# Performance work log

Measured on AMD Instinct MI355X. Metric: run time of the kernel, lower is better.

Reference implementation:

```python
import jax, jax.numpy as jnp
import numpy as np

B, T, D, H, J = 64, 128, 768, 256, 128  # batch, tokens, input_dim, span_hidden_dim, top_injection_dim
PRUNING_RATIO = 2.0


def setup_inputs() -> dict:
    key = jax.random.key(0)
    ks = jax.random.split(key, 12)
    def w(k, shape, fan_in):
        return jax.random.normal(k, shape, jnp.float32) / np.sqrt(fan_in)
    return {
        "inputs": jax.random.normal(ks[0], (B, T, D), jnp.float32),
        "input_mask": jnp.ones((B, T), jnp.int32),
        "top_injection_embedding": jax.random.normal(ks[1], (B, J), jnp.float32),
        # SpanRepAssembly: start / end projections
        "W_start": w(ks[2], (D, H), D), "b_start": jnp.zeros((H,), jnp.float32),
        "W_end": w(ks[3], (D, H), D), "b_end": jnp.zeros((H,), jnp.float32),
        # span_scorer: ReLU -> Linear(H,H) -> ReLU -> Linear(H,1)
        "W_s1": w(ks[4], (H, H), H), "b_s1": jnp.zeros((H,), jnp.float32),
        "W_s2": w(ks[5], (H, 1), H), "b_s2": jnp.zeros((1,), jnp.float32),
        # top injection path
        "W_inj": w(ks[6], (J, H), J), "b_inj": jnp.zeros((H,), jnp.float32),
        "W_sec": w(ks[7], (H, H), H), "b_sec": jnp.zeros((H,), jnp.float32),
        "W_pred": w(ks[8], (H, 1), H), "b_pred": jnp.zeros((1,), jnp.float32),
    }


def reference(inputs, input_mask, top_injection_embedding,
              W_start, b_start, W_end, b_end,
              W_s1, b_s1, W_s2, b_s2,
              W_inj, b_inj, W_sec, b_sec, W_pred, b_pred):
    b, t, _ = inputs.shape
    k_spans = int(PRUNING_RATIO * t)
    # SpanRepAssembly: span_hidden[b, (s,e)] = startProj(x_s) + endProj(x_e), s <= e,
    # flattened start-major (matches start_end_range ordering).
    A = inputs @ W_start + b_start                      # [B,T,H]
    E = inputs @ W_end + b_end                          # [B,T,H]
    s_idx, e_idx = jnp.triu_indices(t)                  # N = T(T+1)/2 spans, row-major
    span_hidden = A[:, s_idx] + E[:, e_idx]             # [B,N,H]
    m = input_mask.astype(jnp.float32)
    span_mask = m[:, s_idx] * m[:, e_idx]               # [B,N]
    # span_scorer MLP over all spans
    h = jax.nn.relu(span_hidden) @ W_s1 + b_s1
    scores = (jax.nn.relu(h) @ W_s2 + b_s2)[..., 0]     # [B,N]
    # SpanPruner: mask invalid spans to -inf, top-k, sort indices, gather
    masked_scores = jnp.where(span_mask > 0, scores, -jnp.inf)
    _, top_idx = jax.lax.top_k(masked_scores, k_spans)  # [B,K]
    top_idx = jnp.sort(top_idx, axis=1)
    top_span_hidden = jnp.take_along_axis(span_hidden, top_idx[:, :, None], axis=1)  # [B,K,H]
    top_span_mask = jnp.take_along_axis(span_mask, top_idx, axis=1)[..., None]       # [B,K,1]
    top_span_scores = jnp.take_along_axis(masked_scores, top_idx, axis=1)[..., None] # [B,K,1]
    top_span_scores = jnp.where(jnp.isinf(top_span_scores), -1.0, top_span_scores)
    # top-injection scoring head
    inj = (top_injection_embedding @ W_inj + b_inj)[:, None, :]      # [B,1,H]
    sec = top_span_hidden @ W_sec + b_sec                            # [B,K,H]
    top_span_logits = jax.nn.relu(inj + sec) @ W_pred + b_pred + top_span_scores  # [B,K,1]
    top_span_probs = jax.nn.sigmoid(top_span_logits) * top_span_mask
    return top_span_probs
```

## Files before the change

### kernel.cpp

```cpp
#include <hip/hip_runtime.h>
#include <hip/hip_bf16.h>
#include <math.h>

#define BB 64
#define T 128
#define DD 768
#define H 256
#define JJ 128
#define NSPAN 8256
#define KTOP 256
#define SCAP 1024
#define MARGIN 0.03f

typedef __attribute__((ext_vector_type(8))) short bf16x8;
typedef __attribute__((ext_vector_type(4))) float f32x4;

__device__ inline unsigned short bfrne(float x) {
    unsigned u = __float_as_uint(x);
    return (unsigned short)((u + 0x7FFFu + ((u >> 16) & 1u)) >> 16);
}

__device__ inline unsigned pk2(float x, float y) {
    float2 f; f.x = x; f.y = y;
    __hip_bfloat162 h = __float22bfloat162_rn(f);
    return *reinterpret_cast<unsigned*>(&h);
}

template<int CTRL>
__device__ __forceinline__ float dpp_add16(float v) {
    return v + __int_as_float(__builtin_amdgcn_update_dpp(
        0, __float_as_int(v), CTRL, 0xF, 0xF, true));
}

__global__ __launch_bounds__(256) void prep_proj_kernel(
    const float* __restrict__ X,
    const float* __restrict__ Wa, const float* __restrict__ ba,
    const float* __restrict__ Wb, const float* __restrict__ bb,
    float* __restrict__ AE,
    int* __restrict__ s_idx, int* __restrict__ e_idx,
    const float* __restrict__ W1, unsigned short* __restrict__ Wpk,
    const float* __restrict__ tie, const float* __restrict__ Winj,
    const float* __restrict__ binj, float* __restrict__ injv)
{
    const int blk = blockIdx.x;
    const int t = threadIdx.x;

    if (blk >= 256) {
        const int pblk = blk - 256;
        if (pblk == 0) {
            if (t < T) {
                int s = t;
                int start = s * T - (s * (s - 1)) / 2;
                int len = T - s;
                for (int i = 0; i < len; ++i) {
                    s_idx[start + i] = s;
                    e_idx[start + i] = s + i;
                }
            }
        } else if (pblk <= 256) {
            int idx = (pblk - 1) * 256 + t;
            int j  = idx & 7;
            int l  = (idx >> 3) & 63;
            int kc = (idx >> 9) & 7;
            int ct = idx >> 12;
            int k = kc * 32 + (l >> 4) * 8 + j;
            int n = ct * 16 + (l & 15);
            Wpk[idx] = bfrne(W1[k * 256 + n]);
        } else {
            int b = pblk - 257;
            __shared__ float tb[JJ];
            if (t < JJ) tb[t] = tie[b * JJ + t];
            __syncthreads();
            float a = binj[t];
            for (int j = 0; j < JJ; ++j)
                a = fmaf(tb[j], Winj[j * H + t], a);
            injv[b * H + t] = a;
        }
        return;
    }

    const int px = blk & 63;
    const int cb = blk >> 6;
    const int m0 = px * 128;
    const float* W    = (cb < 2) ? Wa : Wb;
    const float* bias = (cb < 2) ? ba : bb;
    const int wc0 = (cb & 1) * 128;
    const int oc0 = (cb < 2) ? wc0 : (256 + wc0);

    __shared__ __align__(16) float Xs[128 * 36];
    __shared__ __align__(16) float Wl[32 * 140];

    const int tx = t & 15;
    const int ty = t >> 4;
    const int ty7 = ty & 7;
    const int wro = tx * 8 + ((tx >> 2) << 2);

    const int xrow = t >> 1;
    const int xh   = t & 1;
    const int xsw  = (xrow >> 3) & 7;
    const int wrow = t >> 4;
    const int wi   = t & 15;

    float4 xg[4], w0r[2], w1r[2];
    {
        const float* xp = &X[(size_t)(m0 + xrow) * DD];
#pragma unroll
        for (int q = 0; q < 4; ++q)
            xg[q] = *(const float4*)&xp[(2 * q + xh) * 4];
        const float* wp0 = &W[(size_t)wrow * 256 + wc0 + wi * 8];
        w0r[0] = *(const float4*)&wp0[0]; w0r[1] = *(const float4*)&wp0[4];
        const float* wp1 = &W[(size_t)(wrow + 16) * 256 + wc0 + wi * 8];
        w1r[0] = *(const float4*)&wp1[0]; w1r[1] = *(const float4*)&wp1[4];
    }

    float acc[8][8];
#pragma unroll
    for (int i = 0; i < 8; ++i)
#pragma unroll
        for (int j = 0; j < 8; ++j) acc[i][j] = 0.f;

    for (int it = 0; it < 24; ++it) {
        __syncthreads();
#pragma unroll
        for (int q = 0; q < 4; ++q) {
            const int kb = 2 * q + xh;
            *(float4*)&Xs[xrow * 36 + ((kb ^ xsw) << 2)] = xg[q];
        }
        *(float4*)&Wl[wrow * 140 + wro]            = w0r[0];
        *(float4*)&Wl[wrow * 140 + wro + 4]        = w0r[1];
        *(float4*)&Wl[(wrow + 16) * 140 + wro]     = w1r[0];
        *(float4*)&Wl[(wrow + 16) * 140 + wro + 4] = w1r[1];
        __syncthreads();
        if (it + 1 < 24) {
            const int kk = (it + 1) * 32;
            const float* xp = &X[(size_t)(m0 + xrow) * DD + kk];
#pragma unroll
            for (int q = 0; q < 4; ++q)
                xg[q] = *(const float4*)&xp[(2 * q + xh) * 4];
            const float* wp0 = &W[(size_t)(kk + wrow) * 256 + wc0 + wi * 8];
            w0r[0] = *(const float4*)&wp0[0]; w0r[1] = *(const float4*)&wp0[4];
            const float* wp1 = &W[(size_t)(kk + wrow + 16) * 256 + wc0 + wi * 8];
            w1r[0] = *(const float4*)&wp1[0]; w1r[1] = *(const float4*)&wp1[4];
        }
#pragma unroll
        for (int kb = 0; kb < 8; ++kb) {
            float4 xv[8];
#pragma unroll
            for (int r8 = 0; r8 < 8; ++r8)
                xv[r8] = *(const float4*)&Xs[(ty * 8 + r8) * 36 + ((kb ^ ty7) << 2)];
#pragma unroll
            for (int j = 0; j < 4; ++j) {
                const int k = kb * 4 + j;
                float4 wv0 = *(const float4*)&Wl[k * 140 + wro];
                float4 wv1 = *(const float4*)&Wl[k * 140 + wro + 4];
                float wq[8] = {wv0.x, wv0.y, wv0.z, wv0.w, wv1.x, wv1.y, wv1.z, wv1.w};
#pragma unroll
                for (int r8 = 0; r8 < 8; ++r8) {
                    const float xv1 = j == 0 ? xv[r8].x : j == 1 ? xv[r8].y
                                    : j == 2 ? xv[r8].z : xv[r8].w;
#pragma unroll
                    for (int c = 0; c < 8; ++c)
                        acc[r8][c] = fmaf(xv1, wq[c], acc[r8][c]);
                }
            }
        }
    }

    float bq[8];
#pragma unroll
    for (int j = 0; j < 8; ++j) bq[j] = bias[wc0 + tx * 8 + j];
#pragma unroll
    for (int r8 = 0; r8 < 8; ++r8) {
        const size_t row = m0 + ty * 8 + r8;
        float4 o0, o1;
        o0.x = acc[r8][0] + bq[0]; o0.y = acc[r8][1] + bq[1];
        o0.z = acc[r8][2] + bq[2]; o0.w = acc[r8][3] + bq[3];
        o1.x = acc[r8][4] + bq[4]; o1.y = acc[r8][5] + bq[5];
        o1.z = acc[r8][6] + bq[6]; o1.w = acc[r8][7] + bq[7];
        *(float4*)&AE[row * 512 + oc0 + tx * 8]     = o0;
        *(float4*)&AE[row * 512 + oc0 + tx * 8 + 4] = o1;
    }
}

__global__ __launch_bounds__(512, 4) void approx_kernel(
    const float* __restrict__ AE,
    const unsigned short* __restrict__ Wpk,
    const float* __restrict__ bs1, const float* __restrict__ Ws2,
    const float* __restrict__ bs2g,
    const int* __restrict__ s_idx, const int* __restrict__ e_idx,
    const int* __restrict__ maskp,
    float* __restrict__ scores)
{
    const int bid   = blockIdx.x;
    const int r     = bid & 7;
    const int q     = bid >> 3;
    const int g     = q >> 3;
    const int chunk = q & 7;
    const int b     = g * 8 + r;
    const int tile0 = chunk * 65;
    const int tcnt  = (516 - tile0 < 65) ? (516 - tile0) : 65;

    __shared__ __align__(16) unsigned short rshf[2][8][64][8];
    __shared__ float pslice[2][8][16];

    const int t      = threadIdx.x;
    const int w      = t >> 6;
    const int lane   = t & 63;
    const int lrow16 = lane & 15;
    const int quad   = lane >> 4;

    bf16x8 bfr[2][8];
    float b1c[2], w2c[2];
#pragma unroll
    for (int c = 0; c < 2; ++c) {
#pragma unroll
        for (int kc = 0; kc < 8; ++kc)
            bfr[c][kc] = *(const bf16x8*)&Wpk[((((2 * w + c) * 8 + kc) * 64) + lane) * 8];
        int col = (2 * w + c) * 16 + lrow16;
        b1c[c] = bs1[col];
        w2c[c] = Ws2[col];
    }
    const float bs2v = bs2g[0];

    const float* Abase = AE + (size_t)b * T * 512;
    const int sp   = t >> 5;
    const int km   = t & 31;
    const int kc_s = km >> 2;
    const int q_s  = km & 3;
    const int slot = (q_s * 16 + sp + kc_s) & 63;

    {
        int n = tile0 * 16 + sp;
        int s = s_idx[n], e = e_idx[n];
        const float* Ar = Abase + (size_t)s * 512 + km * 8;
        const float* Er = Abase + (size_t)e * 512 + 256 + km * 8;
        float4 a0 = *(const float4*)&Ar[0];
        float4 a1 = *(const float4*)&Ar[4];
        float4 e0 = *(const float4*)&Er[0];
        float4 e1 = *(const float4*)&Er[4];
        uint4 v;
        v.x = pk2(fmaxf(a0.x + e0.x, 0.f), fmaxf(a0.y + e0.y, 0.f));
        v.y = pk2(fmaxf(a0.z + e0.z, 0.f), fmaxf(a0.w + e0.w, 0.f));
        v.z = pk2(fmaxf(a1.x + e1.x, 0.f), fmaxf(a1.y + e1.y, 0.f));
        v.w = pk2(fmaxf(a1.z + e1.z, 0.f), fmaxf(a1.w + e1.w, 0.f));
        *(uint4*)&rshf[0][kc_s][slot][0] = v;
    }
    int s_nx = 0, e_nx = 0;
    if (tcnt > 1) {
        int n = (tile0 + 1) * 16 + sp;
        s_nx = s_idx[n]; e_nx = e_idx[n];
    }
    __syncthreads();

    for (int tt = 0; tt < tcnt; ++tt) {
        const int cur = tt & 1;
        float4 a0, a1, e0, e1;
        const bool pf = (tt + 1 < tcnt);
        if (pf) {
            const float* Ar = Abase + (size_t)s_nx * 512 + km * 8;
            const float* Er = Abase + (size_t)e_nx * 512 + 256 + km * 8;
            a0 = *(const float4*)&Ar[0];
            a1 = *(const float4*)&Ar[4];
            e0 = *(const float4*)&Er[0];
            e1 = *(const float4*)&Er[4];
        }
        if (tt + 2 < tcnt) {
            int n = (tile0 + tt + 2) * 16 + sp;
            s_nx = s_idx[n]; e_nx = e_idx[n];
        }
        f32x4 acc0 = {0.f, 0.f, 0.f, 0.f};
        f32x4 acc1 = {0.f, 0.f, 0.f, 0.f};
#pragma unroll
        for (int kc = 0; kc < 8; ++kc) {
            bf16x8 a = *(const bf16x8*)&rshf[cur][kc][(lane + kc) & 63][0];
            acc0 = __builtin_amdgcn_mfma_f32_16x16x32_bf16(a, bfr[0][kc], acc0, 0, 0, 0);
            acc1 = __builtin_amdgcn_mfma_f32_16x16x32_bf16(a, bfr[1][kc], acc1, 0, 0, 0);
        }
        float ps[4];
#pragma unroll
        for (int rr = 0; rr < 4; ++rr)
            ps[rr] = fmaxf(acc0[rr] + b1c[0], 0.f) * w2c[0]
                   + fmaxf(acc1[rr] + b1c[1], 0.f) * w2c[1];
#pragma unroll
        for (int rr = 0; rr < 4; ++rr) {
            float v = ps[rr];
            v = dpp_add16<0xB1>(v);
            v = dpp_add16<0x4E>(v);
            v = dpp_add16<0x141>(v);
            v = dpp_add16<0x140>(v);
            ps[rr] = v;
        }
        if (lrow16 == 0) {
            float4 v; v.x = ps[0]; v.y = ps[1]; v.z = ps[2]; v.w = ps[3];
            *(float4*)&pslice[cur][w][quad * 4] = v;
        }
        if (pf) {
            uint4 v;
            v.x = pk2(fmaxf(a0.x + e0.x, 0.f), fmaxf(a0.y + e0.y, 0.f));
            v.y = pk2(fmaxf(a0.z + e0.z, 0.f), fmaxf(a0.w + e0.w, 0.f));
            v.z = pk2(fmaxf(a1.x + e1.x, 0.f), fmaxf(a1.y + e1.y, 0.f));
            v.w = pk2(fmaxf(a1.z + e1.z, 0.f), fmaxf(a1.w + e1.w, 0.f));
            *(uint4*)&rshf[cur ^ 1][kc_s][slot][0] = v;
        }
        __syncthreads();
        if (t < 16) {
            int n = (tile0 + tt) * 16 + t;
            float sc = bs2v;
#pragma unroll
            for (int ww = 0; ww < 8; ++ww) sc += pslice[cur][ww][t];
            int s = s_idx[n], e = e_idx[n];
            bool m = (maskp[b * T + s] != 0) && (maskp[b * T + e] != 0);
            scores[(size_t)b * NSPAN + n] = m ? sc : -INFINITY;
        }
    }
}

__global__ __launch_bounds__(1024) void select_kernel(
    const float* __restrict__ scores,
    int* __restrict__ shortlist, int* __restrict__ slcnt)
{
    const int b = blockIdx.x;
    const int t = threadIdx.x;
    __shared__ unsigned su[NSPAN];
    __shared__ int hist[256];
    __shared__ unsigned s_prefix;
    __shared__ int s_remaining;
    __shared__ int wave_keep[16];

    const float* sc = scores + (size_t)b * NSPAN;
    for (int i = t; i < NSPAN; i += 1024) {
        unsigned ub = __float_as_uint(sc[i]);
        su[i] = (ub & 0x80000000u) ? ~ub : (ub | 0x80000000u);
    }
    __syncthreads();

    unsigned prefix = 0;
    int remaining = KTOP;
    for (int d = 3; d >= 0; --d) {
        if (t < 256) hist[t] = 0;
        __syncthreads();
        const int sh = d * 8;
        for (int i = t; i < NSPAN; i += 1024) {
            unsigned u = su[i];
            bool match = (d == 3) || ((u >> (sh + 8)) == (prefix >> (sh + 8)));
            if (match) atomicAdd(&hist[(u >> sh) & 255], 1);
        }
        __syncthreads();
        if (t == 0) {
            int acc = 0, v = 255;
            for (; v > 0; --v) {
                int h = hist[v];
                if (acc + h >= remaining) break;
                acc += h;
            }
            s_prefix = prefix | ((unsigned)v << sh);
            s_remaining = remaining - acc;
        }
        __syncthreads();
        prefix = s_prefix;
        remaining = s_remaining;
        __syncthreads();
    }

    unsigned ub = (prefix & 0x80000000u) ? (prefix & 0x7FFFFFFFu) : ~prefix;
    float kthf = __uint_as_float(ub);
    float tau = kthf - MARGIN;
    unsigned tb = __float_as_uint(tau);
    unsigned ktau = (tb & 0x80000000u) ? ~tb : (tb | 0x80000000u);

    const int wid = t >> 6, lane = t & 63;
    int base = 0;
    const unsigned long long ltmask = (1ull << lane) - 1ull;
    for (int c0 = 0; c0 < NSPAN; c0 += 1024) {
        int n = c0 + t;
        bool keep = (n < NSPAN) && (su[n] >= ktau);
        unsigned long long bk = __ballot(keep);
        int before = __popcll(bk & ltmask);
        if (lane == 0) wave_keep[wid] = __popcll(bk);
        __syncthreads();
        int kb = base;
        for (int wv = 0; wv < wid; ++wv) kb += wave_keep[wv];
        if (keep) {
            int pos = kb + before;
            if (pos < SCAP) shortlist[b * SCAP + pos] = n;
        }
        for (int wv = 0; wv < 16; ++wv) base += wave_keep[wv];
        __syncthreads();
    }
    if (t == 0) slcnt[b] = base < SCAP ? base : SCAP;
}

__global__ __launch_bounds__(512) void exact_kernel(
    const float* __restrict__ AE,
    const float* __restrict__ Ws1, const float* __restrict__ bs1,
    const float* __restrict__ Ws2, const float* __restrict__ bs2g,
    const int* __restrict__ s_idx, const int* __restrict__ e_idx,
    const int* __restrict__ shortlist, const int* __restrict__ slcnt,
    float* __restrict__ scores)
{
    const int b  = blockIdx.y;
    const int n0 = blockIdx.x * 64;
    const int cntb = slcnt[b];
    if (n0 >= cntb) return;

    __shared__ float rsh[64][36];
    __shared__ float Ws[32][260];
    __shared__ int   ss[64], se[64], nn[64];

    const int t = threadIdx.x;
    if (t < 64) {
        int row = n0 + t;
        int n = 0;
        if (row < cntb) n = shortlist[b * SCAP + row];
        nn[t] = (row < cntb) ? n : -1;
        ss[t] = s_idx[n]; se[t] = e_idx[n];
    }
    __syncthreads();

    const int tx = t & 31;
    const int ty = t >> 5;
    float acc[4][8];
#pragma unroll
    for (int i = 0; i < 4; ++i)
#pragma unroll
        for (int j = 0; j < 8; ++j) acc[i][j] = 0.f;

    const float* Abase = AE + (size_t)b * T * 512;

    for (int kk = 0; kk < 256; kk += 32) {
        __syncthreads();
        {
            int row = t >> 4, q4 = (t & 15) * 4;
#pragma unroll
            for (int q = 0; q < 4; ++q)
                *(float4*)&Ws[row][q4 + q * 64] =
                    *(const float4*)&Ws1[(size_t)(kk + row) * 256 + q4 + q * 64];
        }
        {
            int sp = t >> 3, k4 = (t & 7) * 4;
            const float* Ar = Abase + (size_t)ss[sp] * 512 + kk + k4;
            const float* Er = Abase + (size_t)se[sp] * 512 + 256 + kk + k4;
            float4 a = *(const float4*)Ar;
            float4 e = *(const float4*)Er;
            float4 v;
            v.x = fmaxf(a.x + e.x, 0.f); v.y = fmaxf(a.y + e.y, 0.f);
            v.z = fmaxf(a.z + e.z, 0.f); v.w = fmaxf(a.w + e.w, 0.f);
            *(float4*)&rsh[sp][k4] = v;
        }
        __syncthreads();
#pragma unroll
        for (int k4 = 0; k4 < 32; k4 += 4) {
            float w[4][8];
#pragma unroll
            for (int kq = 0; kq < 4; ++kq) {
                float4 w0 = *(const float4*)&Ws[k4 + kq][tx * 4];
                float4 w1 = *(const float4*)&Ws[k4 + kq][128 + tx * 4];
                w[kq][0] = w0.x; w[kq][1] = w0.y; w[kq][2] = w0.z; w[kq][3] = w0.w;
                w[kq][4] = w1.x; w[kq][5] = w1.y; w[kq][6] = w1.z; w[kq][7] = w1.w;
            }
#pragma unroll
            for (int i = 0; i < 4; ++i) {
                float4 rv = *(const float4*)&rsh[ty * 4 + i][k4];
                float rq[4] = {rv.x, rv.y, rv.z, rv.w};
#pragma unroll
                for (int kq = 0; kq < 4; ++kq)
#pragma unroll
                    for (int j = 0; j < 8; ++j)
                        acc[i][j] = fmaf(rq[kq], w[kq][j], acc[i][j]);
            }
        }
    }

    float b1[8], w2[8];
#pragma unroll
    for (int j = 0; j < 8; ++j) {
        int c = (j < 4) ? (tx * 4 + j) : (128 + tx * 4 + j - 4);
        b1[j] = bs1[c];
        w2[j] = Ws2[c];
    }
    const float bs2v = bs2g[0];
#pragma unroll
    for (int i = 0; i < 4; ++i) {
        int r = ty * 4 + i;
        float p = 0.f;
#pragma unroll
        for (int j = 0; j < 8; ++j)
            p += fmaxf(acc[i][j] + b1[j], 0.f) * w2[j];
#pragma unroll
        for (int off = 16; off > 0; off >>= 1)
            p += __shfl_down(p, off, 32);
        if (tx == 0) {
            int n = nn[r];
            if (n >= 0)
                scores[(size_t)b * NSPAN + n] = p + bs2v;
        }
    }
}

__global__ __launch_bounds__(1024) void topk_kernel(
    const float* __restrict__ scores,
    const int* __restrict__ shortlist, const int* __restrict__ slcnt,
    int* __restrict__ top_idx, float* __restrict__ top_scores)
{
    const int b = blockIdx.x;
    const int t = threadIdx.x;
    const int cnt = slcnt[b];

    __shared__ unsigned su[SCAP];
    __shared__ int sn[SCAP];
    __shared__ int hist[256];
    __shared__ unsigned s_prefix;
    __shared__ int s_remaining;
    __shared__ int wave_eq[16], wave_keep[16];

    for (int i = t; i < cnt; i += 1024) {
        int n = shortlist[b * SCAP + i];
        unsigned ub = __float_as_uint(scores[(size_t)b * NSPAN + n]);
        su[i] = (ub & 0x80000000u) ? ~ub : (ub | 0x80000000u);
        sn[i] = n;
    }
    __syncthreads();

    unsigned prefix = 0;
    int remaining = KTOP;
    for (int d = 3; d >= 0; --d) {
        if (t < 256) hist[t] = 0;
        __syncthreads();
        const int sh = d * 8;
        for (int i = t; i < cnt; i += 1024) {
            unsigned u = su[i];
            bool match = (d == 3) || ((u >> (sh + 8)) == (prefix >> (sh + 8)));
            if (match) atomicAdd(&hist[(u >> sh) & 255], 1);
        }
        __syncthreads();
        if (t == 0) {
            int acc = 0, v = 255;
            for (; v > 0; --v) {
                int h = hist[v];
                if (acc + h >= remaining) break;
                acc += h;
            }
            s_prefix = prefix | ((unsigned)v << sh);
            s_remaining = remaining - acc;
        }
        __syncthreads();
        prefix = s_prefix;
        remaining = s_remaining;
        __syncthreads();
    }
    const unsigned v = prefix;
    const int need_eq = remaining;

    const int wid = t >> 6, lane = t & 63;
    int base_eq = 0, base_keep = 0;
    const unsigned long long ltmask = (1ull << lane) - 1ull;
    for (int c0 = 0; c0 < cnt; c0 += 1024) {
        int i = c0 + t;
        bool valid = i < cnt;
        unsigned u = valid ? su[i] : 0u;
        bool eq = valid && (u == v);
        bool gt = valid && (u > v);
        unsigned long long beq = __ballot(eq);
        int eq_before = __popcll(beq & ltmask);
        if (lane == 0) wave_eq[wid] = __popcll(beq);
        __syncthreads();
        int eqb = base_eq;
        for (int w = 0; w < wid; ++w) eqb += wave_eq[w];
        int eq_rank = eqb + eq_before;
        bool keep = gt || (eq && (eq_rank < need_eq));
        unsigned long long bk = __ballot(keep);
        int keep_before = __popcll(bk & ltmask);
        if (lane == 0) wave_keep[wid] = __popcll(bk);
        __syncthreads();
        int kb = base_keep;
        for (int w = 0; w < wid; ++w) kb += wave_keep[w];
        if (keep) {
            int pos = kb + keep_before;
            top_idx[b * KTOP + pos] = sn[i];
            unsigned fb = (u & 0x80000000u) ? (u & 0x7FFFFFFFu) : ~u;
            float f = __uint_as_float(fb);
            top_scores[b * KTOP + pos] = isinf(f) ? -1.0f : f;
        }
        for (int w = 0; w < 16; ++w) { base_eq += wave_eq[w]; base_keep += wave_keep[w]; }
        __syncthreads();
    }
}

__global__ __launch_bounds__(256) void final_kernel(
    const float* __restrict__ AE,
    const int* __restrict__ s_idx, const int* __restrict__ e_idx,
    const int* __restrict__ maskp,
    const int* __restrict__ top_idx, const float* __restrict__ top_scores,
    const float* __restrict__ injv,
    const float* __restrict__ Wsec, const float* __restrict__ bsec,
    const float* __restrict__ Wpred, const float* __restrict__ bpredg,
    float* __restrict__ out)
{
    const int b = blockIdx.x >> 2;
    const int k0 = (blockIdx.x & 3) * 64;

    __shared__ float sh[64][36];
    __shared__ float Ws[32][260];
    __shared__ int ss[64], se[64];
    __shared__ float msk[64], tsc[64];

    const int t = threadIdx.x;
    if (t < 64) {
        int kidx = k0 + t;
        int n = top_idx[b * KTOP + kidx];
        int s = s_idx[n], e = e_idx[n];
        ss[t] = s; se[t] = e;
        msk[t] = (maskp[b * T + s] != 0 && maskp[b * T + e] != 0) ? 1.f : 0.f;
        tsc[t] = top_scores[b * KTOP + kidx];
    }
    __syncthreads();

    const int tx = t & 31;
    const int ty = t >> 5;
    float acc[8][8];
#pragma unroll
    for (int i = 0; i < 8; ++i)
#pragma unroll
        for (int j = 0; j < 8; ++j) acc[i][j] = 0.f;

    const float* Abase = AE + (size_t)b * T * 512;

    for (int kk = 0; kk < 256; kk += 32) {
        __syncthreads();
        {
            int c4 = (t & 63) * 4, r0 = t >> 6;
#pragma unroll
            for (int r8 = 0; r8 < 8; ++r8) {
                int row = r0 + r8 * 4;
                *(float4*)&Ws[row][c4] =
                    *(const float4*)&Wsec[(size_t)(kk + row) * 256 + c4];
            }
        }
        {
            int sp = t >> 2, k8 = (t & 3) * 8;
            const float* Ar = Abase + (size_t)ss[sp] * 512 + kk + k8;
            const float* Er = Abase + (size_t)se[sp] * 512 + 256 + kk + k8;
#pragma unroll
            for (int q = 0; q < 2; ++q) {
                float4 a = *(const float4*)&Ar[q * 4];
                float4 e = *(const float4*)&Er[q * 4];
                float4 v;
                v.x = a.x + e.x; v.y = a.y + e.y; v.z = a.z + e.z; v.w = a.w + e.w;
                *(float4*)&sh[sp][k8 + q * 4] = v;
            }
        }
        __syncthreads();
#pragma unroll
        for (int k4 = 0; k4 < 32; k4 += 4) {
            float w[4][8];
#pragma unroll
            for (int kq = 0; kq < 4; ++kq) {
                float4 w0 = *(const float4*)&Ws[k4 + kq][tx * 4];
                float4 w1 = *(const float4*)&Ws[k4 + kq][128 + tx * 4];
                w[kq][0] = w0.x; w[kq][1] = w0.y; w[kq][2] = w0.z; w[kq][3] = w0.w;
                w[kq][4] = w1.x; w[kq][5] = w1.y; w[kq][6] = w1.z; w[kq][7] = w1.w;
            }
#pragma unroll
            for (int i = 0; i < 8; ++i) {
                float4 rv = *(const float4*)&sh[ty * 8 + i][k4];
                float rq[4] = {rv.x, rv.y, rv.z, rv.w};
#pragma unroll
                for (int kq = 0; kq < 4; ++kq)
#pragma unroll
                    for (int j = 0; j < 8; ++j)
                        acc[i][j] = fmaf(rq[kq], w[kq][j], acc[i][j]);
            }
        }
    }

    float bsec_r[8], wpred_r[8], injr[8];
#pragma unroll
    for (int j = 0; j < 8; ++j) {
        int c = (j < 4) ? (tx * 4 + j) : (128 + tx * 4 + j - 4);
        bsec_r[j] = bsec[c];
        wpred_r[j] = Wpred[c];
        injr[j] = injv[b * H + c];
    }
    const float bp = bpredg[0];
#pragma unroll
    for (int i = 0; i < 8; ++i) {
        int r = ty * 8 + i;
        float p = 0.f;
#pragma unroll
        for (int j = 0; j < 8; ++j) {
            float sec = acc[i][j] + bsec_r[j];
            p += fmaxf(injr[j] + sec, 0.f) * wpred_r[j];
        }
#pragma unroll
        for (int off = 16; off > 0; off >>= 1)
            p += __shfl_down(p, off, 32);
        if (tx == 0) {
            float logit = p + bp + tsc[r];
            float prob = (1.f / (1.f + expf(-logit))) * msk[r];
            out[b * KTOP + k0 + r] = prob;
        }
    }
}

extern "C" void kernel_launch(void* const* d_in, const int* in_sizes, int n_in,
                              void* d_out, int out_size, void* d_ws, size_t ws_size,
                              hipStream_t stream) {
    const float* inputs  = (const float*)d_in[0];
    const int*   imask   = (const int*)d_in[1];
    const float* tie     = (const float*)d_in[2];
    const float* W_start = (const float*)d_in[3];
    const float* b_start = (const float*)d_in[4];
    const float* W_end   = (const float*)d_in[5];
    const float* b_end   = (const float*)d_in[6];
    const float* W_s1    = (const float*)d_in[7];
    const float* b_s1    = (const float*)d_in[8];
    const float* W_s2    = (const float*)d_in[9];
    const float* b_s2    = (const float*)d_in[10];
    const float* W_inj   = (const float*)d_in[11];
    const float* b_inj   = (const float*)d_in[12];
    const float* W_sec   = (const float*)d_in[13];
    const float* b_sec   = (const float*)d_in[14];
    const float* W_pred  = (const float*)d_in[15];
    const float* b_pred  = (const float*)d_in[16];
    float* out = (float*)d_out;

    float* AE         = (float*)d_ws;
    float* scores     = AE + (size_t)BB * T * 512;
    int*   s_idx      = (int*)(scores + (size_t)BB * NSPAN);
    int*   e_idx      = s_idx + NSPAN;
    int*   top_idx    = e_idx + NSPAN;
    float* top_scores = (float*)(top_idx + BB * KTOP);
    float* injv       = top_scores + BB * KTOP;
    unsigned short* Wpk = (unsigned short*)(injv + BB * H);
    int*   shortlist  = (int*)(Wpk + 65536);
    int*   slcnt      = shortlist + BB * SCAP;

    prep_proj_kernel<<<577, 256, 0, stream>>>(inputs, W_start, b_start, W_end, b_end, AE,
                                              s_idx, e_idx, W_s1, Wpk,
                                              tie, W_inj, b_inj, injv);
    approx_kernel<<<512, 512, 0, stream>>>(AE, Wpk, b_s1, W_s2, b_s2,
                                           s_idx, e_idx, imask, scores);
    select_kernel<<<BB, 1024, 0, stream>>>(scores, shortlist, slcnt);
    exact_kernel<<<dim3(16, BB), 512, 0, stream>>>(AE, W_s1, b_s1, W_s2, b_s2,
                                                   s_idx, e_idx, shortlist, slcnt, scores);
    topk_kernel<<<BB, 1024, 0, stream>>>(scores, shortlist, slcnt, top_idx, top_scores);
    final_kernel<<<BB * 4, 256, 0, stream>>>(AE, s_idx, e_idx, imask, top_idx, top_scores,
                                             injv, W_sec, b_sec, W_pred, b_pred, out);
}
```

Measured before the change: 500.5 us.

## Replace LDS-staged projection GEMM with direct global-to-register double-buffered loads

```diff
diff --git a/kernel.cpp b/kernel.cpp
--- a/kernel.cpp
+++ b/kernel.cpp
@@ -87,96 +87,70 @@
     const int wc0 = (cb & 1) * 128;
     const int oc0 = (cb < 2) ? wc0 : (256 + wc0);
 
-    __shared__ __align__(16) float Xs[128 * 36];
-    __shared__ __align__(16) float Wl[32 * 140];
-
     const int tx = t & 15;
     const int ty = t >> 4;
-    const int ty7 = ty & 7;
-    const int wro = tx * 8 + ((tx >> 2) << 2);
-
-    const int xrow = t >> 1;
-    const int xh   = t & 1;
-    const int xsw  = (xrow >> 3) & 7;
-    const int wrow = t >> 4;
-    const int wi   = t & 15;
-
-    float4 xg[4], w0r[2], w1r[2];
-    {
-        const float* xp = &X[(size_t)(m0 + xrow) * DD];
-#pragma unroll
-        for (int q = 0; q < 4; ++q)
-            xg[q] = *(const float4*)&xp[(2 * q + xh) * 4];
-        const float* wp0 = &W[(size_t)wrow * 256 + wc0 + wi * 8];
-        w0r[0] = *(const float4*)&wp0[0]; w0r[1] = *(const float4*)&wp0[4];
-        const float* wp1 = &W[(size_t)(wrow + 16) * 256 + wc0 + wi * 8];
-        w1r[0] = *(const float4*)&wp1[0]; w1r[1] = *(const float4*)&wp1[4];
-    }
-
+    const int r0 = m0 + ty * 8;
+    const int c0 = wc0 + tx * 8;
+
+    const float* Xb  = X + (size_t)r0 * DD;
+    const float* Wc  = W + c0;
+
+    float4 XA[8], WA[8], XB[8], WB[8];
     float acc[8][8];
 #pragma unroll
     for (int i = 0; i < 8; ++i)
 #pragma unroll
         for (int j = 0; j < 8; ++j) acc[i][j] = 0.f;
 
-    for (int it = 0; it < 24; ++it) {
-        __syncthreads();
-#pragma unroll
-        for (int q = 0; q < 4; ++q) {
-            const int kb = 2 * q + xh;
-            *(float4*)&Xs[xrow * 36 + ((kb ^ xsw) << 2)] = xg[q];
-        }
-        *(float4*)&Wl[wrow * 140 + wro]            = w0r[0];
-        *(float4*)&Wl[wrow * 140 + wro + 4]        = w0r[1];
-        *(float4*)&Wl[(wrow + 16) * 140 + wro]     = w1r[0];
-        *(float4*)&Wl[(wrow + 16) * 140 + wro + 4] = w1r[1];
-        __syncthreads();
-        if (it + 1 < 24) {
-            const int kk = (it + 1) * 32;
-            const float* xp = &X[(size_t)(m0 + xrow) * DD + kk];
-#pragma unroll
-            for (int q = 0; q < 4; ++q)
-                xg[q] = *(const float4*)&xp[(2 * q + xh) * 4];
-            const float* wp0 = &W[(size_t)(kk + wrow) * 256 + wc0 + wi * 8];
-            w0r[0] = *(const float4*)&wp0[0]; w0r[1] = *(const float4*)&wp0[4];
-            const float* wp1 = &W[(size_t)(kk + wrow + 16) * 256 + wc0 + wi * 8];
-            w1r[0] = *(const float4*)&wp1[0]; w1r[1] = *(const float4*)&wp1[4];
-        }
-#pragma unroll
-        for (int kb = 0; kb < 8; ++kb) {
-            float4 xv[8];
-#pragma unroll
-            for (int r8 = 0; r8 < 8; ++r8)
-                xv[r8] = *(const float4*)&Xs[(ty * 8 + r8) * 36 + ((kb ^ ty7) << 2)];
-#pragma unroll
-            for (int j = 0; j < 4; ++j) {
-                const int k = kb * 4 + j;
-                float4 wv0 = *(const float4*)&Wl[k * 140 + wro];
-                float4 wv1 = *(const float4*)&Wl[k * 140 + wro + 4];
-                float wq[8] = {wv0.x, wv0.y, wv0.z, wv0.w, wv1.x, wv1.y, wv1.z, wv1.w};
-#pragma unroll
-                for (int r8 = 0; r8 < 8; ++r8) {
-                    const float xv1 = j == 0 ? xv[r8].x : j == 1 ? xv[r8].y
-                                    : j == 2 ? xv[r8].z : xv[r8].w;
-#pragma unroll
-                    for (int c = 0; c < 8; ++c)
-                        acc[r8][c] = fmaf(xv1, wq[c], acc[r8][c]);
-                }
-            }
-        }
+    auto loadX = [&](float4 (&xr)[8], int kb) {
+        const int kk = kb * 4;
+#pragma unroll
+        for (int r = 0; r < 8; ++r)
+            xr[r] = *(const float4*)&Xb[(size_t)r * DD + kk];
+    };
+    auto loadW = [&](float4 (&wr)[8], int kb) {
+#pragma unroll
+        for (int j = 0; j < 4; ++j) {
+            const float* wp = &Wc[(size_t)(kb * 4 + j) * 256];
+            wr[j * 2]     = *(const float4*)&wp[0];
+            wr[j * 2 + 1] = *(const float4*)&wp[4];
+        }
+    };
+    auto comp = [&](const float4 (&xr)[8], const float4 (&wr)[8]) {
+#pragma unroll
+        for (int j = 0; j < 4; ++j) {
+            const float wq[8] = {wr[j*2].x, wr[j*2].y, wr[j*2].z, wr[j*2].w,
+                                 wr[j*2+1].x, wr[j*2+1].y, wr[j*2+1].z, wr[j*2+1].w};
+#pragma unroll
+            for (int r = 0; r < 8; ++r) {
+                const float xv = (j == 0) ? xr[r].x : (j == 1) ? xr[r].y
+                               : (j == 2) ? xr[r].z : xr[r].w;
+#pragma unroll
+                for (int c = 0; c < 8; ++c)
+                    acc[r][c] = fmaf(xv, wq[c], acc[r][c]);
+            }
+        }
+    };
+
+    loadX(XA, 0); loadW(WA, 0);
+    for (int kb = 0; kb < 192; kb += 2) {
+        loadX(XB, kb + 1); loadW(WB, kb + 1);
+        comp(XA, WA);
+        if (kb + 2 < 192) { loadX(XA, kb + 2); loadW(WA, kb + 2); }
+        comp(XB, WB);
     }
 
     float bq[8];
 #pragma unroll
     for (int j = 0; j < 8; ++j) bq[j] = bias[wc0 + tx * 8 + j];
 #pragma unroll
-    for (int r8 = 0; r8 < 8; ++r8) {
-        const size_t row = m0 + ty * 8 + r8;
+    for (int r = 0; r < 8; ++r) {
+        const size_t row = r0 + r;
         float4 o0, o1;
-        o0.x = acc[r8][0] + bq[0]; o0.y = acc[r8][1] + bq[1];
-        o0.z = acc[r8][2] + bq[2]; o0.w = acc[r8][3] + bq[3];
-        o1.x = acc[r8][4] + bq[4]; o1.y = acc[r8][5] + bq[5];
-        o1.z = acc[r8][6] + bq[6]; o1.w = acc[r8][7] + bq[7];
+        o0.x = acc[r][0] + bq[0]; o0.y = acc[r][1] + bq[1];
+        o0.z = acc[r][2] + bq[2]; o0.w = acc[r][3] + bq[3];
+        o1.x = acc[r][4] + bq[4]; o1.y = acc[r][5] + bq[5];
+        o1.z = acc[r][6] + bq[6]; o1.w = acc[r][7] + bq[7];
         *(float4*)&AE[row * 512 + oc0 + tx * 8]     = o0;
         *(float4*)&AE[row * 512 + oc0 + tx * 8 + 4] = o1;
     }
```

Result: faster. 477.7 us (-4.5%).
